# Kernel optimization log

Measured on AMD Instinct MI355X. Metric: run time of the kernel, lower is better.

The kernel has to match this reference:

```python
import jax, jax.numpy as jnp
import numpy as np

B, FEAT, Q, L, H_ENC, H_DEC = 256, 64, 16, 2, 128, 256


def _apply_1q(state, U, q):
    # state: [B, 2,2,...,2] (Q qubit axes); U: [B,2,2] complex64
    s = jnp.moveaxis(state, 1 + q, 1)
    shp = s.shape
    s2 = s.reshape(shp[0], 2, -1)
    s2 = jnp.einsum('bij,bjr->bir', U, s2)
    return jnp.moveaxis(s2.reshape(shp), 1, 1 + q)


def _apply_cnot(state, c, t):
    # flip target axis on the control=1 slice
    c0 = jnp.take(state, 0, axis=1 + c)
    c1 = jnp.take(state, 1, axis=1 + c)
    t_ax = 1 + t if t < c else t  # target axis index after removing control axis
    c1 = jnp.flip(c1, axis=t_ax)
    return jnp.stack([c0, c1], axis=1 + c)


def _u3(theta, phi, lam):
    # combined Rz(lam) @ Ry(phi) @ Rx(theta); inputs [B] -> [B,2,2] complex64
    j = jnp.complex64(1j)
    ct, st = jnp.cos(theta / 2), jnp.sin(theta / 2)
    cp, sp = jnp.cos(phi / 2), jnp.sin(phi / 2)
    Rx = jnp.stack([jnp.stack([ct + 0j, -j * st], -1),
                    jnp.stack([-j * st, ct + 0j], -1)], -2)
    Ry = jnp.stack([jnp.stack([cp + 0j, -sp + 0j], -1),
                    jnp.stack([sp + 0j, cp + 0j], -1)], -2)
    em, ep = jnp.exp(-j * lam / 2), jnp.exp(j * lam / 2)
    zero = jnp.zeros_like(em)
    Rz = jnp.stack([jnp.stack([em, zero], -1),
                    jnp.stack([zero, ep], -1)], -2)
    return jnp.einsum('bij,bjk,bkl->bil', Rz, Ry, Rx).astype(jnp.complex64)


def setup_inputs() -> dict:
    key = jax.random.key(0)
    ks = jax.random.split(key, 6)

    def xavier(k, shape):
        lim = float(np.sqrt(6.0 / (shape[0] + shape[1])))
        return jax.random.uniform(k, shape, jnp.float32, -lim, lim)

    return {
        'x': jax.random.normal(ks[0], (B, FEAT), jnp.float32),
        'W1': xavier(ks[1], (FEAT, H_ENC)), 'b1': jnp.zeros((H_ENC,), jnp.float32),
        'W2': xavier(ks[2], (H_ENC, L * Q * 3)), 'b2': jnp.zeros((L * Q * 3,), jnp.float32),
        'scaling': jnp.ones((Q,), jnp.float32),
        'Wd1': xavier(ks[3], (2 ** Q, H_DEC)), 'bd1': jnp.zeros((H_DEC,), jnp.float32),
        'Wd2': xavier(ks[4], (H_DEC, FEAT)), 'bd2': jnp.zeros((FEAT,), jnp.float32),
    }


def reference(x, W1, b1, W2, b2, scaling, Wd1, bd1, Wd2, bd2):
    batch = x.shape[0]
    nq = scaling.shape[0]
    nl = W2.shape[1] // (nq * 3)
    # classical encoder -> quantum rotation angles
    h = jax.nn.relu(x @ W1 + b1)
    p = jnp.tanh(h @ W2 + b2).reshape(batch, nl, nq, 3)
    p = p * scaling[None, None, :, None] * jnp.pi  # theta/phi/lambda scaled by pi
    # batched statevector simulation, |0...0> init
    state = jnp.zeros((batch, 2 ** nq), jnp.complex64).at[:, 0].set(1.0)
    state = state.reshape((batch,) + (2,) * nq)
    for l in range(nl):
        for q in range(nq):
            U = _u3(p[:, l, q, 0], p[:, l, q, 1], p[:, l, q, 2])
            state = _apply_1q(state, U, q)
        if l < nl - 1:
            for q in range(nq - 1):
                state = _apply_cnot(state, q, q + 1)
            state = _apply_cnot(state, nq - 1, 0)
    probs = (jnp.real(state) ** 2 + jnp.imag(state) ** 2).reshape(batch, -1)
    # classical decoder
    out = jax.nn.relu(jax.nn.relu(probs @ Wd1 + bd1) @ Wd2 + bd2)
    return out
```

## Files before the change

kernel.cpp:

```cpp
#include <hip/hip_runtime.h>
#include <hip/hip_fp16.h>

#define PI_F 3.14159265358979323846f

typedef __attribute__((ext_vector_type(8))) _Float16 f16x8;
typedef __attribute__((ext_vector_type(16))) float f32x16;
typedef __attribute__((ext_vector_type(2))) float v2f;

__device__ __forceinline__ v2f pfma(v2f a, v2f b, v2f c) {
    return __builtin_elementwise_fma(a, b, c);
}
__device__ __forceinline__ v2f vswap(v2f a) { return __builtin_shufflevector(a, a, 1, 0); }
__device__ __forceinline__ v2f vsplat(float x) { v2f r; r.x = x; r.y = x; return r; }
__device__ __forceinline__ v2f mkc(v2f u) { v2f r; r.x = -u.y; r.y = u.y; return r; }
__device__ __forceinline__ v2f cmul(v2f a, v2f b) {
    return pfma(mkc(a), vswap(b), vsplat(a.x) * b);
}

__device__ __forceinline__ unsigned f2bf_rn(float x) {
    unsigned u = __float_as_uint(x);
    return (u + 0x7fffu + ((u >> 16) & 1u)) >> 16;
}

union H8 { int4 i4; f16x8 v; };

__device__ __forceinline__ void gll16(const void* g, void* l) {
    __builtin_amdgcn_global_load_lds(
        (const __attribute__((address_space(1))) void*)g,
        (__attribute__((address_space(3))) void*)l, 16, 0, 0);
}

union PreLds {
    struct {
        float xr[64]; float h[128]; float ang[96];
        v2f vL[32];
        v2f uL[64];
        _Float16 lR[256*8];
        _Float16 lL[512*8];
    } e;
    _Float16 wt[64][134];
};

__global__ __launch_bounds__(256) void k_pre(
        const float* __restrict__ x, const float* __restrict__ W1,
        const float* __restrict__ b1, const float* __restrict__ W2,
        const float* __restrict__ b2, const float* __restrict__ scaling,
        const float* __restrict__ Wd1, _Float16* __restrict__ Wt,
        _Float16* __restrict__ A) {
    __shared__ PreLds lds;
    const int t = threadIdx.x;
    if (blockIdx.x >= 256) {
        const int cb = blockIdx.x - 256;
        const int kb = (cb >> 2) * 128;
        const int nb = (cb & 3) * 64;
        unsigned* wtw = (unsigned*)&lds.wt[0][0];
        #pragma unroll
        for (int it = 0; it < 4; ++it) {
            int idx = t + it*256;
            int kr2 = idx >> 4;
            int nc4 = (idx & 15) * 4;
            const float* src = Wd1 + (size_t)(kb + 2*kr2)*256 + nb + nc4;
            float4 w0 = *(const float4*)src;
            float4 w1 = *(const float4*)(src + 256);
            #pragma unroll
            for (int j = 0; j < 4; ++j) {
                float a0 = (j==0?w0.x:j==1?w0.y:j==2?w0.z:w0.w) * 64.f;
                float a1 = (j==0?w1.x:j==1?w1.y:j==2?w1.z:w1.w) * 64.f;
                __half2 hh = __floats2half2_rn(a0, a1);
                unsigned u; __builtin_memcpy(&u, &hh, 4);
                wtw[(nc4 + j)*67 + kr2] = u;
            }
        }
        __syncthreads();
        #pragma unroll
        for (int it = 0; it < 4; ++it) {
            int idx = t + it*256;
            int n = idx >> 4, u = idx & 15;
            int4 hh = *(const int4*)&lds.wt[n][u*8];
            *(int4*)(Wt + ((size_t)(nb + n) << 16) + kb + u*8) = hh;
        }
        return;
    }
    const int b = blockIdx.x;
    if (t < 64) lds.e.xr[t] = x[b*64 + t];
    __syncthreads();
    if (t < 128) {
        float acc = b1[t];
        #pragma unroll 8
        for (int f = 0; f < 64; ++f) acc = fmaf(lds.e.xr[f], W1[f*128 + t], acc);
        lds.e.h[t] = fmaxf(acc, 0.f);
    }
    __syncthreads();
    if (t < 96) {
        float acc = b2[t];
        #pragma unroll 8
        for (int f = 0; f < 128; ++f) acc = fmaf(lds.e.h[f], W2[f*96 + t], acc);
        int q = (t/3) & 15;
        lds.e.ang[t] = tanhf(acc) * scaling[q] * PI_F;
    }
    __syncthreads();
    if (t < 32) {
        int l = t >> 4, q = t & 15;
        const float* a = lds.e.ang + l*48 + q*3;
        float st, ct, sp, cp, sl, cl;
        sincosf(a[0]*0.5f, &st, &ct);
        sincosf(a[1]*0.5f, &sp, &cp);
        sincosf(a[2]*0.5f, &sl, &cl);
        float2 A00 = make_float2( cp*ct,  sp*st);
        float2 A01 = make_float2(-sp*ct, -cp*st);
        float2 A10 = make_float2( sp*ct, -cp*st);
        float2 A11 = make_float2( cp*ct, -sp*st);
        float2 e0 = make_float2(cl, -sl), e1 = make_float2(cl, sl);
        v2f r00; r00.x = e0.x*A00.x - e0.y*A00.y; r00.y = e0.x*A00.y + e0.y*A00.x;
        v2f r01; r01.x = e0.x*A01.x - e0.y*A01.y; r01.y = e0.x*A01.y + e0.y*A01.x;
        v2f r10; r10.x = e1.x*A10.x - e1.y*A10.y; r10.y = e1.x*A10.y + e1.y*A10.x;
        v2f r11; r11.x = e1.x*A11.x - e1.y*A11.y; r11.y = e1.x*A11.y + e1.y*A11.x;
        if (l == 0) {
            lds.e.vL[q*2 + 0] = r00;
            lds.e.vL[q*2 + 1] = r10;
        } else {
            lds.e.uL[q*4 + 0] = r00; lds.e.uL[q*4 + 1] = r01;
            lds.e.uL[q*4 + 2] = r10; lds.e.uL[q*4 + 3] = r11;
        }
    }
    __syncthreads();
    #define AP(p, s) lds.e.vL[(15-(p))*2 + (s)]
    #define GG(p, zv, yv) lds.e.uL[(15-(p))*4 + (zv)*2 + (yv)]
    const float SL = 32.f;
    v2f Lg[2][2];
    {
        int z0 = t & 1, z1 = (t >> 1) & 1;
        #pragma unroll
        for (int g = 0; g < 2; ++g)
            #pragma unroll
            for (int y = 0; y < 2; ++y)
                Lg[g][y] = cmul(cmul(GG(0, z0, g), AP(0, g ^ y)), GG(1, z1, y));
        #pragma unroll
        for (int p = 2; p <= 7; ++p) {
            int zp = (t >> p) & 1;
            #pragma unroll
            for (int g = 0; g < 2; ++g) {
                v2f s0 = cmul(Lg[g][0], AP(p-1, 0)) + cmul(Lg[g][1], AP(p-1, 1));
                v2f s1 = cmul(Lg[g][0], AP(p-1, 1)) + cmul(Lg[g][1], AP(p-1, 0));
                Lg[g][0] = cmul(s0, GG(p, zp, 0));
                Lg[g][1] = cmul(s1, GG(p, zp, 1));
            }
        }
    }
    v2f Rg[2][2];
    {
        int z15 = (t >> 7) & 1;
        #pragma unroll
        for (int g = 0; g < 2; ++g)
            #pragma unroll
            for (int y14 = 0; y14 < 2; ++y14)
                Rg[g][y14] = cmul(cmul(AP(14, y14 ^ g),     AP(15, g)),     GG(15, z15, 0))
                           + cmul(cmul(AP(14, y14 ^ 1 ^ g), AP(15, 1 ^ g)), GG(15, z15, 1));
        #pragma unroll
        for (int p = 14; p >= 8; --p) {
            int zp = (t >> (p - 8)) & 1;
            #pragma unroll
            for (int g = 0; g < 2; ++g) {
                v2f t0 = cmul(GG(p, zp, 0), Rg[g][0]);
                v2f t1 = cmul(GG(p, zp, 1), Rg[g][1]);
                v2f n0 = cmul(AP(p-1, 0), t0) + cmul(AP(p-1, 1), t1);
                v2f n1 = cmul(AP(p-1, 1), t0) + cmul(AP(p-1, 0), t1);
                Rg[g][0] = n0; Rg[g][1] = n1;
            }
        }
    }
    #undef AP
    #undef GG
    {
        float lre[4] = {Lg[0][0].x, Lg[0][1].x, Lg[1][0].x, Lg[1][1].x};
        float lim[4] = {Lg[0][0].y, Lg[0][1].y, Lg[1][0].y, Lg[1][1].y};
        float rre[4] = {Rg[0][0].x, Rg[0][1].x, Rg[1][0].x, Rg[1][1].x};
        float rim[4] = {Rg[0][0].y, Rg[0][1].y, Rg[1][0].y, Rg[1][1].y};
        H8 hre, him, hr;
        #pragma unroll
        for (int k = 0; k < 4; ++k) {
            hre.v[k]   = (_Float16)(SL * lre[k]);
            hre.v[4+k] = (_Float16)(-SL * lim[k]);
            him.v[k]   = (_Float16)(SL * lim[k]);
            him.v[4+k] = (_Float16)(SL * lre[k]);
            hr.v[k]    = (_Float16)(SL * rre[k]);
            hr.v[4+k]  = (_Float16)(SL * rim[k]);
        }
        *(int4*)&lds.e.lR[t*8]         = hr.i4;
        *(int4*)&lds.e.lL[t*8]         = hre.i4;
        *(int4*)&lds.e.lL[(256+t)*8]   = him.i4;
    }
    __syncthreads();
    {
        const int wave = t >> 6, lane = t & 63, h2 = lane >> 5, l32 = lane & 31;
        f16x8 zf = {};
        _Float16* Aout = A + ((size_t)b << 16);
        #pragma unroll
        for (int mt2 = 0; mt2 < 2; ++mt2) {
            const int zh0 = (wave*2 + mt2)*32;
            f16x8 af = h2 ? zf : *(const f16x8*)&lds.e.lR[(zh0 + l32)*8];
            #pragma unroll
            for (int j = 0; j < 8; ++j) {
                f16x8 bre = h2 ? zf : *(const f16x8*)&lds.e.lL[(j*32 + l32)*8];
                f16x8 bim = h2 ? zf : *(const f16x8*)&lds.e.lL[(256 + j*32 + l32)*8];
                f32x16 zc = {};
                f32x16 dre = __builtin_amdgcn_mfma_f32_32x32x16_f16(af, bre, zc, 0, 0, 0);
                f32x16 dim = __builtin_amdgcn_mfma_f32_32x32x16_f16(af, bim, zc, 0, 0, 0);
                #pragma unroll
                for (int q = 0; q < 16; ++q) {
                    float p = fmaf(dre[q], dre[q], dim[q]*dim[q]) * 0.00390625f;
                    int row = zh0 + 4*h2 + (q & 3) + 8*(q >> 2);
                    Aout[row*256 + j*32 + l32] = (_Float16)p;
                }
            }
        }
    }
}

__global__ __launch_bounds__(256, 4) void k_gemm(
        const _Float16* __restrict__ A, const _Float16* __restrict__ Bt,
        unsigned short* __restrict__ partial) {
    __shared__ _Float16 lA[128*64];
    __shared__ _Float16 lB[128*64];
    const int id = blockIdx.x;
    const int ks = (id & 7) | ((id >> 5) << 3);
    const int p  = (id >> 3) & 3;
    const int nt = p >> 1, mt = p & 1;
    const int k0 = ks*256, n0 = nt*128, m0 = mt*128;
    const int tid = threadIdx.x, wave = tid >> 6, lane = tid & 63;
    const int mw = wave >> 1, nw = wave & 1;
    const int h = lane >> 5, l32 = lane & 31;
    f32x16 acc[2][2] = {};
    for (int s = 0; s < 4; ++s) {
        const int kb = k0 + s*64;
        #pragma unroll
        for (int i = 0; i < 4; ++i) {
            int ia = wave*4 + i;
            int r = ia*8 + (lane >> 3);
            int cch = (lane & 7) ^ (r & 7);
            gll16(A  + (size_t)(m0 + r)*65536 + kb + cch*8, &lA[ia*512]);
            gll16(Bt + (size_t)(n0 + r)*65536 + kb + cch*8, &lB[ia*512]);
        }
        __syncthreads();
        #pragma unroll
        for (int kk = 0; kk < 4; ++kk) {
            const int ch = kk*2 + h;
            f16x8 af[2], bf[2];
            #pragma unroll
            for (int xx = 0; xx < 2; ++xx) {
                int rA = mw*64 + xx*32 + l32;
                af[xx] = *(const f16x8*)&lA[rA*64 + ((ch ^ (rA & 7)) << 3)];
                int rB = nw*64 + xx*32 + l32;
                bf[xx] = *(const f16x8*)&lB[rB*64 + ((ch ^ (rB & 7)) << 3)];
            }
            #pragma unroll
            for (int i = 0; i < 2; ++i)
                #pragma unroll
                for (int jj = 0; jj < 2; ++jj)
                    acc[i][jj] = __builtin_amdgcn_mfma_f32_32x32x16_f16(af[i], bf[jj], acc[i][jj], 0, 0, 0);
        }
        __syncthreads();
    }
    unsigned short* pp = partial + (size_t)ks*65536;
    #pragma unroll
    for (int i = 0; i < 2; ++i) {
        #pragma unroll
        for (int jj = 0; jj < 2; ++jj) {
            int n = n0 + nw*64 + jj*32 + l32;
            int mb = m0 + mw*64 + i*32 + 4*h;
            #pragma unroll
            for (int q = 0; q < 16; ++q) {
                int m = mb + (q & 3) + 8*(q >> 2);
                pp[m*256 + n] = (unsigned short)f2bf_rn(acc[i][jj][q]);
            }
        }
    }
}

__global__ __launch_bounds__(256) void k_final(
        const unsigned short* __restrict__ partial, const float* __restrict__ bd1,
        const float* __restrict__ Wd2, const float* __restrict__ bd2,
        float* __restrict__ out) {
    __shared__ float row[256];
    const int m = blockIdx.x, t = threadIdx.x;
    {
        const unsigned short* p = partial + m*256 + t;
        float s = 0.f;
        #pragma unroll 32
        for (int kc = 0; kc < 256; ++kc)
            s += __uint_as_float(((unsigned)p[(size_t)kc*65536]) << 16);
        const float SC = 1.f / 262144.f;
        row[t] = fmaxf(fmaf(s, SC, bd1[t]), 0.f);
    }
    __syncthreads();
    if (t < 64) {
        float o = bd2[t];
        #pragma unroll 8
        for (int n = 0; n < 256; ++n) o = fmaf(row[n], Wd2[n*64 + t], o);
        out[m*64 + t] = fmaxf(o, 0.f);
    }
}

extern "C" void kernel_launch(void* const* d_in, const int* in_sizes, int n_in,
                              void* d_out, int out_size, void* d_ws, size_t ws_size,
                              hipStream_t stream) {
    const float* x       = (const float*)d_in[0];
    const float* W1      = (const float*)d_in[1];
    const float* b1      = (const float*)d_in[2];
    const float* W2      = (const float*)d_in[3];
    const float* b2      = (const float*)d_in[4];
    const float* scaling = (const float*)d_in[5];
    const float* Wd1     = (const float*)d_in[6];
    const float* bd1     = (const float*)d_in[7];
    const float* Wd2     = (const float*)d_in[8];
    const float* bd2     = (const float*)d_in[9];
    float* out = (float*)d_out;

    char* ws = (char*)d_ws;
    const size_t MB = 1024*1024;
    _Float16* A  = (_Float16*)(ws + 4*MB);
    _Float16* Wt = (_Float16*)(ws + 36*MB);
    unsigned short* partial = (unsigned short*)(ws + 68*MB);

    hipLaunchKernelGGL(k_pre, dim3(2304), dim3(256), 0, stream,
                       x, W1, b1, W2, b2, scaling, Wd1, Wt, A);
    hipLaunchKernelGGL(k_gemm, dim3(1024), dim3(256), 0, stream, A, Wt, partial);
    hipLaunchKernelGGL(k_final, dim3(256), dim3(256), 0, stream,
                       partial, bd1, Wd2, bd2, out);
}
```

Measured before the change: 165.6 us.

## Fuse Wd1 fp16 conversion into GEMM and make partial layout contiguous per row

Drops the separate Wd1 transpose/convert blocks from k_pre. The GEMM now loads raw fp32 Wd1 tiles straight into LDS and converts them to scaled fp16 fragments on the fly, which removes a 32MB fp16 write and its re-read. The partial-sum layout is changed to [m][ks][n] so k_final reads contiguous 16-byte vectors and reduces through LDS, instead of making strided scalar loads. In exchange the GEMM reads twice the bytes for B (fp32), needs more LDS, drops occupancy from 4 to 3, and does extra conversion ALU work inside the inner loop.

```diff
diff --git a/kernel.cpp b/kernel.cpp
--- a/kernel.cpp
+++ b/kernel.cpp
@@ -22,7 +22,7 @@
     return (u + 0x7fffu + ((u >> 16) & 1u)) >> 16;
 }
 
-union H8 { int4 i4; f16x8 v; };
+union H8 { int4 i4; unsigned w[4]; f16x8 v; };
 
 __device__ __forceinline__ void gll16(const void* g, void* l) {
     __builtin_amdgcn_global_load_lds(
@@ -30,78 +30,42 @@
         (__attribute__((address_space(3))) void*)l, 16, 0, 0);
 }
 
-union PreLds {
-    struct {
-        float xr[64]; float h[128]; float ang[96];
-        v2f vL[32];
-        v2f uL[64];
-        _Float16 lR[256*8];
-        _Float16 lL[512*8];
-    } e;
-    _Float16 wt[64][134];
+struct PreLds {
+    float xr[64]; float h[128]; float ang[96];
+    v2f vL[32];
+    v2f uL[64];
+    _Float16 lR[256*8];
+    _Float16 lL[512*8];
 };
 
 __global__ __launch_bounds__(256) void k_pre(
         const float* __restrict__ x, const float* __restrict__ W1,
         const float* __restrict__ b1, const float* __restrict__ W2,
         const float* __restrict__ b2, const float* __restrict__ scaling,
-        const float* __restrict__ Wd1, _Float16* __restrict__ Wt,
         _Float16* __restrict__ A) {
     __shared__ PreLds lds;
     const int t = threadIdx.x;
-    if (blockIdx.x >= 256) {
-        const int cb = blockIdx.x - 256;
-        const int kb = (cb >> 2) * 128;
-        const int nb = (cb & 3) * 64;
-        unsigned* wtw = (unsigned*)&lds.wt[0][0];
-        #pragma unroll
-        for (int it = 0; it < 4; ++it) {
-            int idx = t + it*256;
-            int kr2 = idx >> 4;
-            int nc4 = (idx & 15) * 4;
-            const float* src = Wd1 + (size_t)(kb + 2*kr2)*256 + nb + nc4;
-            float4 w0 = *(const float4*)src;
-            float4 w1 = *(const float4*)(src + 256);
-            #pragma unroll
-            for (int j = 0; j < 4; ++j) {
-                float a0 = (j==0?w0.x:j==1?w0.y:j==2?w0.z:w0.w) * 64.f;
-                float a1 = (j==0?w1.x:j==1?w1.y:j==2?w1.z:w1.w) * 64.f;
-                __half2 hh = __floats2half2_rn(a0, a1);
-                unsigned u; __builtin_memcpy(&u, &hh, 4);
-                wtw[(nc4 + j)*67 + kr2] = u;
-            }
-        }
-        __syncthreads();
-        #pragma unroll
-        for (int it = 0; it < 4; ++it) {
-            int idx = t + it*256;
-            int n = idx >> 4, u = idx & 15;
-            int4 hh = *(const int4*)&lds.wt[n][u*8];
-            *(int4*)(Wt + ((size_t)(nb + n) << 16) + kb + u*8) = hh;
-        }
-        return;
-    }
     const int b = blockIdx.x;
-    if (t < 64) lds.e.xr[t] = x[b*64 + t];
+    if (t < 64) lds.xr[t] = x[b*64 + t];
     __syncthreads();
     if (t < 128) {
         float acc = b1[t];
         #pragma unroll 8
-        for (int f = 0; f < 64; ++f) acc = fmaf(lds.e.xr[f], W1[f*128 + t], acc);
-        lds.e.h[t] = fmaxf(acc, 0.f);
+        for (int f = 0; f < 64; ++f) acc = fmaf(lds.xr[f], W1[f*128 + t], acc);
+        lds.h[t] = fmaxf(acc, 0.f);
     }
     __syncthreads();
     if (t < 96) {
         float acc = b2[t];
         #pragma unroll 8
-        for (int f = 0; f < 128; ++f) acc = fmaf(lds.e.h[f], W2[f*96 + t], acc);
+        for (int f = 0; f < 128; ++f) acc = fmaf(lds.h[f], W2[f*96 + t], acc);
         int q = (t/3) & 15;
-        lds.e.ang[t] = tanhf(acc) * scaling[q] * PI_F;
+        lds.ang[t] = tanhf(acc) * scaling[q] * PI_F;
     }
     __syncthreads();
     if (t < 32) {
         int l = t >> 4, q = t & 15;
-        const float* a = lds.e.ang + l*48 + q*3;
+        const float* a = lds.ang + l*48 + q*3;
         float st, ct, sp, cp, sl, cl;
         sincosf(a[0]*0.5f, &st, &ct);
         sincosf(a[1]*0.5f, &sp, &cp);
@@ -116,16 +80,16 @@
         v2f r10; r10.x = e1.x*A10.x - e1.y*A10.y; r10.y = e1.x*A10.y + e1.y*A10.x;
         v2f r11; r11.x = e1.x*A11.x - e1.y*A11.y; r11.y = e1.x*A11.y + e1.y*A11.x;
         if (l == 0) {
-            lds.e.vL[q*2 + 0] = r00;
-            lds.e.vL[q*2 + 1] = r10;
+            lds.vL[q*2 + 0] = r00;
+            lds.vL[q*2 + 1] = r10;
         } else {
-            lds.e.uL[q*4 + 0] = r00; lds.e.uL[q*4 + 1] = r01;
-            lds.e.uL[q*4 + 2] = r10; lds.e.uL[q*4 + 3] = r11;
-        }
-    }
-    __syncthreads();
-    #define AP(p, s) lds.e.vL[(15-(p))*2 + (s)]
-    #define GG(p, zv, yv) lds.e.uL[(15-(p))*4 + (zv)*2 + (yv)]
+            lds.uL[q*4 + 0] = r00; lds.uL[q*4 + 1] = r01;
+            lds.uL[q*4 + 2] = r10; lds.uL[q*4 + 3] = r11;
+        }
+    }
+    __syncthreads();
+    #define AP(p, s) lds.vL[(15-(p))*2 + (s)]
+    #define GG(p, zv, yv) lds.uL[(15-(p))*4 + (zv)*2 + (yv)]
     const float SL = 32.f;
     v2f Lg[2][2];
     {
@@ -186,9 +150,9 @@
             hr.v[k]    = (_Float16)(SL * rre[k]);
             hr.v[4+k]  = (_Float16)(SL * rim[k]);
         }
-        *(int4*)&lds.e.lR[t*8]         = hr.i4;
-        *(int4*)&lds.e.lL[t*8]         = hre.i4;
-        *(int4*)&lds.e.lL[(256+t)*8]   = him.i4;
+        *(int4*)&lds.lR[t*8]         = hr.i4;
+        *(int4*)&lds.lL[t*8]         = hre.i4;
+        *(int4*)&lds.lL[(256+t)*8]   = him.i4;
     }
     __syncthreads();
     {
@@ -198,11 +162,11 @@
         #pragma unroll
         for (int mt2 = 0; mt2 < 2; ++mt2) {
             const int zh0 = (wave*2 + mt2)*32;
-            f16x8 af = h2 ? zf : *(const f16x8*)&lds.e.lR[(zh0 + l32)*8];
+            f16x8 af = h2 ? zf : *(const f16x8*)&lds.lR[(zh0 + l32)*8];
             #pragma unroll
             for (int j = 0; j < 8; ++j) {
-                f16x8 bre = h2 ? zf : *(const f16x8*)&lds.e.lL[(j*32 + l32)*8];
-                f16x8 bim = h2 ? zf : *(const f16x8*)&lds.e.lL[(256 + j*32 + l32)*8];
+                f16x8 bre = h2 ? zf : *(const f16x8*)&lds.lL[(j*32 + l32)*8];
+                f16x8 bim = h2 ? zf : *(const f16x8*)&lds.lL[(256 + j*32 + l32)*8];
                 f32x16 zc = {};
                 f32x16 dre = __builtin_amdgcn_mfma_f32_32x32x16_f16(af, bre, zc, 0, 0, 0);
                 f32x16 dim = __builtin_amdgcn_mfma_f32_32x32x16_f16(af, bim, zc, 0, 0, 0);
@@ -217,11 +181,11 @@
     }
 }
 
-__global__ __launch_bounds__(256, 4) void k_gemm(
-        const _Float16* __restrict__ A, const _Float16* __restrict__ Bt,
+__global__ __launch_bounds__(256, 3) void k_gemm(
+        const _Float16* __restrict__ A, const float* __restrict__ Wd1,
         unsigned short* __restrict__ partial) {
     __shared__ _Float16 lA[128*64];
-    __shared__ _Float16 lB[128*64];
+    __shared__ float lB[64*128];
     const int id = blockIdx.x;
     const int ks = (id & 7) | ((id >> 5) << 3);
     const int p  = (id >> 3) & 3;
@@ -238,8 +202,14 @@
             int ia = wave*4 + i;
             int r = ia*8 + (lane >> 3);
             int cch = (lane & 7) ^ (r & 7);
-            gll16(A  + (size_t)(m0 + r)*65536 + kb + cch*8, &lA[ia*512]);
-            gll16(Bt + (size_t)(n0 + r)*65536 + kb + cch*8, &lB[ia*512]);
+            gll16(A + (size_t)(m0 + r)*65536 + kb + cch*8, &lA[ia*512]);
+        }
+        #pragma unroll
+        for (int i = 0; i < 8; ++i) {
+            int ib = wave*8 + i;
+            int kr = ib*2 + (lane >> 5);
+            int nc = (lane & 31) * 4;
+            gll16(Wd1 + (size_t)(kb + kr)*256 + n0 + nc, &lB[ib*256]);
         }
         __syncthreads();
         #pragma unroll
@@ -250,8 +220,20 @@
             for (int xx = 0; xx < 2; ++xx) {
                 int rA = mw*64 + xx*32 + l32;
                 af[xx] = *(const f16x8*)&lA[rA*64 + ((ch ^ (rA & 7)) << 3)];
-                int rB = nw*64 + xx*32 + l32;
-                bf[xx] = *(const f16x8*)&lB[rB*64 + ((ch ^ (rB & 7)) << 3)];
+            }
+            #pragma unroll
+            for (int j2 = 0; j2 < 2; ++j2) {
+                const int col = nw*64 + j2*32 + l32;
+                const float* bp = &lB[(kk*16 + h*8)*128 + col];
+                H8 bh;
+                #pragma unroll
+                for (int d = 0; d < 4; ++d) {
+                    float f0 = bp[(2*d)*128]   * 64.f;
+                    float f1 = bp[(2*d+1)*128] * 64.f;
+                    __half2 hh = __floats2half2_rn(f0, f1);
+                    __builtin_memcpy(&bh.w[d], &hh, 4);
+                }
+                bf[j2] = bh.v;
             }
             #pragma unroll
             for (int i = 0; i < 2; ++i)
@@ -261,7 +243,6 @@
         }
         __syncthreads();
     }
-    unsigned short* pp = partial + (size_t)ks*65536;
     #pragma unroll
     for (int i = 0; i < 2; ++i) {
         #pragma unroll
@@ -271,7 +252,7 @@
             #pragma unroll
             for (int q = 0; q < 16; ++q) {
                 int m = mb + (q & 3) + 8*(q >> 2);
-                pp[m*256 + n] = (unsigned short)f2bf_rn(acc[i][jj][q]);
+                partial[((size_t)m*256 + ks)*256 + n] = (unsigned short)f2bf_rn(acc[i][jj][q]);
             }
         }
     }
@@ -281,14 +262,30 @@
         const unsigned short* __restrict__ partial, const float* __restrict__ bd1,
         const float* __restrict__ Wd2, const float* __restrict__ bd2,
         float* __restrict__ out) {
+    __shared__ float red[8][256];
     __shared__ float row[256];
     const int m = blockIdx.x, t = threadIdx.x;
-    {
-        const unsigned short* p = partial + m*256 + t;
+    const int kgrp = t >> 5, nb8 = (t & 31) * 8;
+    const unsigned short* base = partial + ((size_t)m << 16);
+    float v[8] = {0.f, 0.f, 0.f, 0.f, 0.f, 0.f, 0.f, 0.f};
+    #pragma unroll 8
+    for (int j = 0; j < 32; ++j) {
+        int ksr = kgrp + 8*j;
+        int4 d = *(const int4*)(base + ksr*256 + nb8);
+        unsigned w[4]; __builtin_memcpy(w, &d, 16);
+        #pragma unroll
+        for (int wd = 0; wd < 4; ++wd) {
+            v[2*wd]   += __uint_as_float(w[wd] << 16);
+            v[2*wd+1] += __uint_as_float(w[wd] & 0xffff0000u);
+        }
+    }
+    #pragma unroll
+    for (int i = 0; i < 8; ++i) red[kgrp][nb8 + i] = v[i];
+    __syncthreads();
+    {
         float s = 0.f;
-        #pragma unroll 32
-        for (int kc = 0; kc < 256; ++kc)
-            s += __uint_as_float(((unsigned)p[(size_t)kc*65536]) << 16);
+        #pragma unroll
+        for (int g = 0; g < 8; ++g) s += red[g][t];
         const float SC = 1.f / 262144.f;
         row[t] = fmaxf(fmaf(s, SC, bd1[t]), 0.f);
     }
@@ -318,13 +315,12 @@
 
     char* ws = (char*)d_ws;
     const size_t MB = 1024*1024;
-    _Float16* A  = (_Float16*)(ws + 4*MB);
-    _Float16* Wt = (_Float16*)(ws + 36*MB);
+    _Float16* A = (_Float16*)(ws + 4*MB);
     unsigned short* partial = (unsigned short*)(ws + 68*MB);
 
-    hipLaunchKernelGGL(k_pre, dim3(2304), dim3(256), 0, stream,
-                       x, W1, b1, W2, b2, scaling, Wd1, Wt, A);
-    hipLaunchKernelGGL(k_gemm, dim3(1024), dim3(256), 0, stream, A, Wt, partial);
+    hipLaunchKernelGGL(k_pre, dim3(256), dim3(256), 0, stream,
+                       x, W1, b1, W2, b2, scaling, A);
+    hipLaunchKernelGGL(k_gemm, dim3(1024), dim3(256), 0, stream, A, Wd1, partial);
     hipLaunchKernelGGL(k_final, dim3(256), dim3(256), 0, stream,
                        partial, bd1, Wd2, bd2, out);
 }
```

New measurement: 170.4 us. 1.03x slower.
